# Performance work log

Measured on AMD Instinct MI355X. Metric: run time of the kernel, lower is better.

## Reference

```python
import jax, jax.numpy as jnp
import numpy as np

B, N, D = 2, 4096, 512   # batch, tokens (64x64 latent), query_dim
H, DH = 8, 64            # heads, dim_head; inner_dim = H*DH = 512


def setup_inputs() -> dict:
    key = jax.random.key(0)
    ks = jax.random.split(key, 6)
    s = lambda fan_in: 1.0 / np.sqrt(fan_in)
    x = jax.random.normal(ks[0], (B, N, D), dtype=jnp.float32)
    Wq = jax.random.uniform(ks[1], (D, H * DH), jnp.float32, -s(D), s(D))
    Wk = jax.random.uniform(ks[2], (D, H * DH), jnp.float32, -s(D), s(D))
    Wv = jax.random.uniform(ks[3], (D, H * DH), jnp.float32, -s(D), s(D))
    Wo = jax.random.uniform(ks[4], (H * DH, D), jnp.float32, -s(H * DH), s(H * DH))
    bo = jax.random.uniform(ks[5], (D,), jnp.float32, -s(H * DH), s(H * DH))
    return {"x": x, "Wq": Wq, "Wk": Wk, "Wv": Wv, "Wo": Wo, "bo": bo}


def reference(x, Wq, Wk, Wv, Wo, bo):
    # Self-attention (context = x). Projections (no bias).
    q = x @ Wq  # [B, N, H*DH]
    k = x @ Wk
    v = x @ Wv
    split = lambda t: t.reshape(B, N, H, DH).transpose(0, 2, 1, 3)  # [B, H, N, DH]
    q, k, v = split(q), split(k), split(v)
    scale = DH ** -0.5
    # fp32 upcast for scores (ATTN_PRECISION == 'fp32' path)
    sim = jnp.einsum('bhid,bhjd->bhij', q.astype(jnp.float32), k.astype(jnp.float32)) * scale
    attn = jax.nn.softmax(sim, axis=-1).astype(v.dtype)
    out = jnp.einsum('bhij,bhjd->bhid', attn, v)           # [B, H, N, DH]
    out = out.transpose(0, 2, 1, 3).reshape(B, N, H * DH)  # [B, N, H*DH]
    return out @ Wo + bo  # to_out Linear (dropout=0)
```

## Files before the change

kernel.cpp:

```cpp
#include <hip/hip_runtime.h>
#include <hip/hip_bf16.h>
#include <stdint.h>


typedef short short8 __attribute__((ext_vector_type(8)));
typedef float f32x4 __attribute__((ext_vector_type(4)));
typedef float f32x16 __attribute__((ext_vector_type(16)));

#define QK_SCALE 0.18033688011112042f
#define M3(a,b,c) fmaxf(fmaxf((a),(b)),(c))

static __device__ __forceinline__ unsigned short f32_to_bf16(float f) {
    union { float f; uint32_t u; } v; v.f = f;
    uint32_t u = v.u;
    u += 0x7FFFu + ((u >> 16) & 1u);
    return (unsigned short)(u >> 16);
}

static __device__ __forceinline__ uint32_t cvt_pk_bf16(float lo, float hi) {
    uint32_t r;
    asm("v_cvt_pk_bf16_f32 %0, %1, %2" : "=v"(r) : "v"(lo), "v"(hi));
    return r;
}

static __device__ __forceinline__ int swz(int row, int byte_in_row) {
    return row * 128 + (byte_in_row ^ ((row & 7) << 4));
}

static __device__ __forceinline__ void gload16(const void* g, void* l) {
    __builtin_amdgcn_global_load_lds(
        (const __attribute__((address_space(1))) unsigned int*)g,
        (__attribute__((address_space(3))) unsigned int*)l, 16, 0, 0);
}

union PAU { uint32_t d[4]; short8 v; };

__global__ __launch_bounds__(256) void convert_weights(
    const float* __restrict__ Wq, const float* __restrict__ Wk,
    const float* __restrict__ Wv, const float* __restrict__ Wo,
    unsigned short* __restrict__ wt)
{
    __shared__ float lds[64][65];
    const int mat = blockIdx.z;
    const float* W = (mat == 0) ? Wq : (mat == 1) ? Wk : (mat == 2) ? Wv : Wo;
    const float scale = (mat == 0) ? QK_SCALE : 1.0f;
    unsigned short* out = wt + (size_t)mat * 512 * 512;
    const int k0 = blockIdx.y * 64, n0 = blockIdx.x * 64;
    for (int i = 0; i < 16; i++) {
        int idx = threadIdx.x + i * 256;
        int kl = idx >> 6, nl = idx & 63;
        lds[kl][nl] = W[(size_t)(k0 + kl) * 512 + n0 + nl];
    }
    __syncthreads();
    for (int i = 0; i < 16; i++) {
        int idx = threadIdx.x + i * 256;
        int nr = idx >> 6, kc = idx & 63;
        out[(size_t)(n0 + nr) * 512 + k0 + kc] = f32_to_bf16(lds[kc][nr] * scale);
    }
}

__global__ __launch_bounds__(256) void convert_x(
    const float* __restrict__ x, unsigned short* __restrict__ xbf)
{
    const int idx = (blockIdx.x * 256 + threadIdx.x) * 8;
    float4 f0 = *reinterpret_cast<const float4*>(x + idx);
    float4 f1 = *reinterpret_cast<const float4*>(x + idx + 4);
    short8 v;
    v[0] = (short)f32_to_bf16(f0.x); v[1] = (short)f32_to_bf16(f0.y);
    v[2] = (short)f32_to_bf16(f0.z); v[3] = (short)f32_to_bf16(f0.w);
    v[4] = (short)f32_to_bf16(f1.x); v[5] = (short)f32_to_bf16(f1.y);
    v[6] = (short)f32_to_bf16(f1.z); v[7] = (short)f32_to_bf16(f1.w);
    *reinterpret_cast<short8*>(xbf + idx) = v;
}

__global__ __launch_bounds__(256, 2) void proj_gemm(
    const unsigned short* __restrict__ xbf,
    const unsigned short* __restrict__ wt,
    unsigned short* __restrict__ q_ws,
    unsigned short* __restrict__ k_ws,
    unsigned short* __restrict__ vt_ws)
{
    __shared__ __attribute__((aligned(16))) char smem[65536];
    const int which = blockIdx.z;
    const unsigned short* W = wt + (size_t)which * 512 * 512;
    const int m0 = blockIdx.y * 128, n0 = blockIdx.x * 128;
    const int tid = threadIdx.x, lane = tid & 63, wid = tid >> 6;
    const int wm = (wid >> 1) * 64, wn = (wid & 1) * 64;
    const int rsub = lane >> 3;
    const int cb = ((lane & 7) ^ rsub) << 4;

    f32x4 acc[4][4];
#pragma unroll
    for (int i = 0; i < 4; i++)
#pragma unroll
        for (int j = 0; j < 4; j++) acc[i][j] = (f32x4){0.f, 0.f, 0.f, 0.f};

#define PSTAGE(KT, BUF)                                                           \
    {                                                                             \
        const int kk0_ = (KT) * 64;                                               \
        _Pragma("unroll")                                                         \
        for (int cj = 0; cj < 4; cj++) {                                          \
            const int chunk = wid * 4 + cj;                                       \
            const int row = chunk * 8 + rsub;                                     \
            gload16((const char*)xbf + ((size_t)(m0 + row) * 512 + kk0_) * 2 + cb,\
                    smem + (BUF) * 32768 + chunk * 1024);                         \
            gload16((const char*)W + ((size_t)(n0 + row) * 512 + kk0_) * 2 + cb,  \
                    smem + (BUF) * 32768 + 16384 + chunk * 1024);                 \
        }                                                                         \
    }

    PSTAGE(0, 0);
    __syncthreads();

    for (int kt = 0; kt < 8; kt++) {
        const int cur = kt & 1;
        if (kt + 1 < 8) PSTAGE(kt + 1, cur ^ 1);
        unsigned short* ldsA = (unsigned short*)(smem + cur * 32768);
        unsigned short* ldsB = ldsA + 8192;
#pragma unroll
        for (int ks = 0; ks < 2; ks++) {
            const int kb = ks * 64 + (lane >> 4) * 16;
            short8 a[4], b[4];
#pragma unroll
            for (int m = 0; m < 4; m++)
                a[m] = *reinterpret_cast<short8*>(ldsA + (swz(wm + m * 16 + (lane & 15), kb) >> 1));
#pragma unroll
            for (int n = 0; n < 4; n++)
                b[n] = *reinterpret_cast<short8*>(ldsB + (swz(wn + n * 16 + (lane & 15), kb) >> 1));
            __builtin_amdgcn_s_setprio(1);
#pragma unroll
            for (int m = 0; m < 4; m++)
#pragma unroll
                for (int n = 0; n < 4; n++)
                    acc[m][n] = __builtin_amdgcn_mfma_f32_16x16x32_bf16(a[m], b[n], acc[m][n], 0, 0, 0);
            __builtin_amdgcn_s_setprio(0);
        }
        __syncthreads();
    }
#pragma unroll
    for (int m = 0; m < 4; m++)
#pragma unroll
        for (int n = 0; n < 4; n++)
#pragma unroll
            for (int r = 0; r < 4; r++) {
                int mr = m0 + wm + m * 16 + (lane >> 4) * 4 + r;
                int nc = n0 + wn + n * 16 + (lane & 15);
                unsigned short hv = f32_to_bf16(acc[m][n][r]);
                int b = mr >> 12, tok = mr & 4095;
                int h = nc >> 6, d = nc & 63;
                size_t bh = (size_t)(b * 8 + h);
                if (which == 2) {
                    vt_ws[(bh * 64 + d) * 4096 + tok] = hv;
                } else {
                    unsigned short* dst = (which == 0) ? q_ws : k_ws;
                    dst[(bh * 4096 + tok) * 64 + d] = hv;
                }
            }
}

__global__ __launch_bounds__(512, 4) void attn_kernel(
    const unsigned short* __restrict__ q_ws,
    const unsigned short* __restrict__ k_ws,
    const unsigned short* __restrict__ vt_ws,
    unsigned short* __restrict__ o_ws)
{
    __shared__ __attribute__((aligned(16))) char smem[65536];
    const int bh = blockIdx.y;
    const int q0 = blockIdx.x * 128;
    const int tid = threadIdx.x, lane = tid & 63, wid = tid >> 6;
    const int g = wid >> 2, sw = wid & 3;
    const int lo = lane & 31, hi = lane >> 5;
    const unsigned short* Qb = q_ws + (size_t)bh * 4096 * 64;
    const unsigned short* Kb = k_ws + (size_t)bh * 4096 * 64 + (size_t)g * 2048 * 64;
    const unsigned short* Vb = vt_ws + (size_t)bh * 64 * 4096 + g * 2048;

    char* gbase = smem + g * 32768;

    short8 qf[4];
    const int qrow = q0 + sw * 32 + lo;
#pragma unroll
    for (int s = 0; s < 4; s++)
        qf[s] = *reinterpret_cast<const short8*>(Qb + (size_t)qrow * 64 + s * 16 + hi * 8);

    f32x16 zv;
#pragma unroll
    for (int i = 0; i < 16; i++) zv[i] = 0.f;
    f32x16 acc[2];
    acc[0] = zv; acc[1] = zv;
    float m_run = -3e38f, l_run = 0.f;

    const int rsub = lane >> 3;
    const int cb = ((lane & 7) ^ rsub) << 4;

#define STAGE(TT, BUF)                                                          \
    {                                                                           \
        const int kv0_ = (TT) * 64;                                             \
        _Pragma("unroll")                                                       \
        for (int j = 0; j < 2; j++) {                                           \
            const int chunk = sw * 2 + j;                                       \
            const int row0 = chunk * 8;                                         \
            gload16((const char*)Kb + (size_t)(kv0_ + row0 + rsub) * 128 + cb,  \
                    gbase + (BUF) * 16384 + chunk * 1024);                      \
            gload16((const char*)Vb + (size_t)(row0 + rsub) * 8192 +            \
                        (size_t)kv0_ * 2 + cb,                                  \
                    gbase + (BUF) * 16384 + 8192 + chunk * 1024);               \
        }                                                                       \
    }

    STAGE(0, 0);
    __syncthreads();

    for (int t = 0; t < 32; t++) {
        const int cur = t & 1;
        if (t + 1 < 32) STAGE(t + 1, cur ^ 1);
        unsigned short* ldsK = (unsigned short*)(gbase + cur * 16384);
        unsigned short* ldsV = ldsK + 4096;

        f32x16 p[2];
        p[0] = zv; p[1] = zv;
        __builtin_amdgcn_s_setprio(1);
#pragma unroll
        for (int tt = 0; tt < 2; tt++)
#pragma unroll
            for (int s = 0; s < 4; s++) {
                short8 kf = *reinterpret_cast<short8*>(&ldsK[swz(tt * 32 + lo, s * 32 + hi * 16) >> 1]);
                p[tt] = __builtin_amdgcn_mfma_f32_32x32x16_bf16(kf, qf[s], p[tt], 0, 0, 0);
            }
        __builtin_amdgcn_s_setprio(0);

        float pm;
        {
            float a0 = M3(p[0][0], p[0][1], p[0][2]);
            float b0 = M3(p[0][3], p[0][4], p[0][5]);
            float c0 = M3(p[0][6], p[0][7], p[0][8]);
            float d0 = M3(p[0][9], p[0][10], p[0][11]);
            float e0 = M3(p[0][12], p[0][13], p[0][14]);
            float a1 = M3(p[1][0], p[1][1], p[1][2]);
            float b1 = M3(p[1][3], p[1][4], p[1][5]);
            float c1 = M3(p[1][6], p[1][7], p[1][8]);
            float d1 = M3(p[1][9], p[1][10], p[1][11]);
            float e1 = M3(p[1][12], p[1][13], p[1][14]);
            float f0 = fmaxf(p[0][15], p[1][15]);
            float x0 = M3(a0, b0, c0), x1 = M3(d0, e0, f0), x2 = M3(a1, b1, c1), x3 = M3(d1, e1, x1);
            pm = M3(x0, x2, x3);
        }
        pm = fmaxf(pm, __shfl_xor(pm, 32, 64));
        if (!__all(pm <= m_run + 8.0f)) {
            float mn = fmaxf(m_run, pm);
            float scl = __builtin_amdgcn_exp2f(m_run - mn);
            acc[0] *= scl; acc[1] *= scl;
            l_run *= scl;
            m_run = mn;
        }
        float s0 = 0.f, s1 = 0.f, s2 = 0.f, s3 = 0.f;
#pragma unroll
        for (int tt = 0; tt < 2; tt++)
#pragma unroll
            for (int i = 0; i < 16; i += 4) {
                float e0 = __builtin_amdgcn_exp2f(p[tt][i] - m_run);
                float e1 = __builtin_amdgcn_exp2f(p[tt][i + 1] - m_run);
                float e2 = __builtin_amdgcn_exp2f(p[tt][i + 2] - m_run);
                float e3 = __builtin_amdgcn_exp2f(p[tt][i + 3] - m_run);
                p[tt][i] = e0; p[tt][i + 1] = e1; p[tt][i + 2] = e2; p[tt][i + 3] = e3;
                s0 += e0; s1 += e1; s2 += e2; s3 += e3;
            }
        float ps = (s0 + s1) + (s2 + s3);
        ps += __shfl_xor(ps, 32, 64);
        l_run += ps;

        short8 pa[4];
#pragma unroll
        for (int tt = 0; tt < 2; tt++) {
            uint32_t w0 = cvt_pk_bf16(p[tt][0],  p[tt][1]);
            uint32_t w1 = cvt_pk_bf16(p[tt][2],  p[tt][3]);
            uint32_t w2 = cvt_pk_bf16(p[tt][4],  p[tt][5]);
            uint32_t w3 = cvt_pk_bf16(p[tt][6],  p[tt][7]);
            uint32_t w4 = cvt_pk_bf16(p[tt][8],  p[tt][9]);
            uint32_t w5 = cvt_pk_bf16(p[tt][10], p[tt][11]);
            uint32_t w6 = cvt_pk_bf16(p[tt][12], p[tt][13]);
            uint32_t w7 = cvt_pk_bf16(p[tt][14], p[tt][15]);
            auto r02 = __builtin_amdgcn_permlane32_swap(w0, w2, false, false);
            auto r13 = __builtin_amdgcn_permlane32_swap(w1, w3, false, false);
            auto r46 = __builtin_amdgcn_permlane32_swap(w4, w6, false, false);
            auto r57 = __builtin_amdgcn_permlane32_swap(w5, w7, false, false);
            PAU ua, ub;
            ua.d[0] = r02[0]; ua.d[1] = r13[0]; ua.d[2] = r02[1]; ua.d[3] = r13[1];
            ub.d[0] = r46[0]; ub.d[1] = r57[0]; ub.d[2] = r46[1]; ub.d[3] = r57[1];
            pa[2 * tt]     = ua.v;
            pa[2 * tt + 1] = ub.v;
        }

        __builtin_amdgcn_s_setprio(1);
#pragma unroll
        for (int dt = 0; dt < 2; dt++)
#pragma unroll
            for (int s = 0; s < 4; s++) {
                short8 vf = *reinterpret_cast<short8*>(&ldsV[swz(dt * 32 + lo, s * 32 + hi * 16) >> 1]);
                acc[dt] = __builtin_amdgcn_mfma_f32_32x32x16_bf16(vf, pa[s], acc[dt], 0, 0, 0);
            }
        __builtin_amdgcn_s_setprio(0);

        __syncthreads();
    }

    float* accbuf = (float*)smem;
    float* mlbuf  = (float*)(smem + 32768);
    if (g == 0) {
        float* ab = accbuf + sw * 2048;
#pragma unroll
        for (int dt = 0; dt < 2; dt++)
#pragma unroll
            for (int r = 0; r < 16; r++) {
                int d = dt * 32 + (r & 3) + 8 * (r >> 2) + 4 * hi;
                ab[d * 32 + lo] = acc[dt][r];
            }
        if (hi == 0) {
            mlbuf[sw * 64 + lo] = m_run;
            mlbuf[sw * 64 + 32 + lo] = l_run;
        }
    }
    __syncthreads();
    if (g == 1) {
        float m0 = mlbuf[sw * 64 + lo], l0 = mlbuf[sw * 64 + 32 + lo];
        float mn = fmaxf(m0, m_run);
        float a0 = __builtin_amdgcn_exp2f(m0 - mn);
        float a1 = __builtin_amdgcn_exp2f(m_run - mn);
        float rl = __builtin_amdgcn_rcpf(a0 * l0 + a1 * l_run);
        const float* ab = accbuf + sw * 2048;
        char* eb = smem + 33792 + sw * 4096;
#pragma unroll
        for (int dt = 0; dt < 2; dt++)
#pragma unroll
            for (int r = 0; r < 16; r++) {
                int d = dt * 32 + (r & 3) + 8 * (r >> 2) + 4 * hi;
                float o = (a0 * ab[d * 32 + lo] + a1 * acc[dt][r]) * rl;
                *(unsigned short*)(eb + swz(lo, d * 2)) = f32_to_bf16(o);
            }
        const int b = bh >> 3, h = bh & 7;
#pragma unroll
        for (int j = 0; j < 4; j++) {
            int c = lane + 64 * j;
            int row = c >> 3, cc = c & 7;
            short8 v = *reinterpret_cast<short8*>(eb + swz(row, cc * 16));
            int tok = q0 + sw * 32 + row;
            *reinterpret_cast<short8*>(o_ws + ((size_t)(b * 4096 + tok)) * 512 + h * 64 + cc * 8) = v;
        }
    }
}

__global__ __launch_bounds__(256, 2) void out_gemm(
    const unsigned short* __restrict__ o_ws,
    const unsigned short* __restrict__ wot,
    const float* __restrict__ bo,
    float* __restrict__ out)
{
    __shared__ __attribute__((aligned(16))) char smem[65536];
    const int m0 = blockIdx.y * 128, n0 = blockIdx.x * 128;
    const int tid = threadIdx.x, lane = tid & 63, wid = tid >> 6;
    const int wm = (wid >> 1) * 64, wn = (wid & 1) * 64;
    const int rsub = lane >> 3;
    const int cb = ((lane & 7) ^ rsub) << 4;

    f32x4 acc[4][4];
#pragma unroll
    for (int i = 0; i < 4; i++)
#pragma unroll
        for (int j = 0; j < 4; j++) acc[i][j] = (f32x4){0.f, 0.f, 0.f, 0.f};

#define OSTAGE(KT, BUF)                                                            \
    {                                                                              \
        const int kk0_ = (KT) * 64;                                                \
        _Pragma("unroll")                                                          \
        for (int cj = 0; cj < 4; cj++) {                                           \
            const int chunk = wid * 4 + cj;                                        \
            const int row = chunk * 8 + rsub;                                      \
            gload16((const char*)o_ws + ((size_t)(m0 + row) * 512 + kk0_) * 2 + cb,\
                    smem + (BUF) * 32768 + chunk * 1024);                          \
            gload16((const char*)wot + ((size_t)(n0 + row) * 512 + kk0_) * 2 + cb, \
                    smem + (BUF) * 32768 + 16384 + chunk * 1024);                  \
        }                                                                          \
    }

    OSTAGE(0, 0);
    __syncthreads();

    for (int kt = 0; kt < 8; kt++) {
        const int cur = kt & 1;
        if (kt + 1 < 8) OSTAGE(kt + 1, cur ^ 1);
        unsigned short* ldsA = (unsigned short*)(smem + cur * 32768);
        unsigned short* ldsB = ldsA + 8192;
#pragma unroll
        for (int ks = 0; ks < 2; ks++) {
            const int kb = ks * 64 + (lane >> 4) * 16;
            short8 a[4], b[4];
#pragma unroll
            for (int m = 0; m < 4; m++)
                a[m] = *reinterpret_cast<short8*>(ldsA + (swz(wm + m * 16 + (lane & 15), kb) >> 1));
#pragma unroll
            for (int n = 0; n < 4; n++)
                b[n] = *reinterpret_cast<short8*>(ldsB + (swz(wn + n * 16 + (lane & 15), kb) >> 1));
            __builtin_amdgcn_s_setprio(1);
#pragma unroll
            for (int m = 0; m < 4; m++)
#pragma unroll
                for (int n = 0; n < 4; n++)
                    acc[m][n] = __builtin_amdgcn_mfma_f32_16x16x32_bf16(a[m], b[n], acc[m][n], 0, 0, 0);
            __builtin_amdgcn_s_setprio(0);
        }
        __syncthreads();
    }
#pragma unroll
    for (int n = 0; n < 4; n++) {
        const int nc = n0 + wn + n * 16 + (lane & 15);
        const float bias = bo[nc];
#pragma unroll
        for (int m = 0; m < 4; m++)
#pragma unroll
            for (int r = 0; r < 4; r++) {
                int mr = m0 + wm + m * 16 + (lane >> 4) * 4 + r;
                out[(size_t)mr * 512 + nc] = acc[m][n][r] + bias;
            }
    }
}

extern "C" void kernel_launch(void* const* d_in, const int* in_sizes, int n_in,
                              void* d_out, int out_size, void* d_ws, size_t ws_size,
                              hipStream_t stream)
{
    const float* x  = (const float*)d_in[0];
    const float* Wq = (const float*)d_in[1];
    const float* Wk = (const float*)d_in[2];
    const float* Wv = (const float*)d_in[3];
    const float* Wo = (const float*)d_in[4];
    const float* bo = (const float*)d_in[5];
    float* out = (float*)d_out;

    char* ws = (char*)d_ws;
    unsigned short* wt    = (unsigned short*)(ws);
    unsigned short* q_ws  = (unsigned short*)(ws + (size_t)(2)  * 1024 * 1024);
    unsigned short* k_ws  = (unsigned short*)(ws + (size_t)(10) * 1024 * 1024);
    unsigned short* vt_ws = (unsigned short*)(ws + (size_t)(18) * 1024 * 1024);
    unsigned short* xbf   = (unsigned short*)(ws + (size_t)(26) * 1024 * 1024);
    unsigned short* o_ws  = xbf;

    convert_weights<<<dim3(8, 8, 4), 256, 0, stream>>>(Wq, Wk, Wv, Wo, wt);
    convert_x<<<dim3(2048), 256, 0, stream>>>(x, xbf);
    proj_gemm<<<dim3(4, 64, 3), 256, 0, stream>>>(xbf, wt, q_ws, k_ws, vt_ws);
    attn_kernel<<<dim3(32, 16), 512, 0, stream>>>(q_ws, k_ws, vt_ws, o_ws);
    out_gemm<<<dim3(4, 64), 256, 0, stream>>>(o_ws, wt + (size_t)3 * 512 * 512, bo, out);
}
```

Measured before the change: 140.2 us.

## Process two 32-row query tiles per wave to reuse K/V fragments

Each wave now handles 64 query rows (two 32-row sub-tiles) instead of 32, so every K and V fragment read from LDS feeds two MFMAs. The block covers 256 queries and the grid becomes 256 one-dimensional blocks, with a remapped block-to-(bh, q0) order that interleaves heads. This halves K/V global and LDS traffic per query but doubles accumulator and score registers, lowering launch bounds occupancy from 4 to 2 blocks per CU. There are also only 256 blocks, which may underfill the GPU's compute units.

```diff
diff --git a/kernel.cpp b/kernel.cpp
--- a/kernel.cpp
+++ b/kernel.cpp
@@ -158,15 +158,132 @@
             }
 }
 
-__global__ __launch_bounds__(512, 4) void attn_kernel(
+static __device__ __forceinline__ void softmax_step(
+    f32x16* p, float& m_run, float& l_run, f32x16* acc, short8* pa)
+{
+    float pm;
+    {
+        float a0 = M3(p[0][0], p[0][1], p[0][2]);
+        float b0 = M3(p[0][3], p[0][4], p[0][5]);
+        float c0 = M3(p[0][6], p[0][7], p[0][8]);
+        float d0 = M3(p[0][9], p[0][10], p[0][11]);
+        float e0 = M3(p[0][12], p[0][13], p[0][14]);
+        float a1 = M3(p[1][0], p[1][1], p[1][2]);
+        float b1 = M3(p[1][3], p[1][4], p[1][5]);
+        float c1 = M3(p[1][6], p[1][7], p[1][8]);
+        float d1 = M3(p[1][9], p[1][10], p[1][11]);
+        float e1 = M3(p[1][12], p[1][13], p[1][14]);
+        float f0 = fmaxf(p[0][15], p[1][15]);
+        float x0 = M3(a0, b0, c0), x1 = M3(d0, e0, f0), x2 = M3(a1, b1, c1), x3 = M3(d1, e1, x1);
+        pm = M3(x0, x2, x3);
+    }
+    pm = fmaxf(pm, __shfl_xor(pm, 32, 64));
+    if (!__all(pm <= m_run + 8.0f)) {
+        float mn = fmaxf(m_run, pm);
+        float scl = __builtin_amdgcn_exp2f(m_run - mn);
+        acc[0] *= scl; acc[1] *= scl;
+        l_run *= scl;
+        m_run = mn;
+    }
+    float s0 = 0.f, s1 = 0.f, s2 = 0.f, s3 = 0.f;
+#pragma unroll
+    for (int tt = 0; tt < 2; tt++)
+#pragma unroll
+        for (int i = 0; i < 16; i += 4) {
+            float e0 = __builtin_amdgcn_exp2f(p[tt][i] - m_run);
+            float e1 = __builtin_amdgcn_exp2f(p[tt][i + 1] - m_run);
+            float e2 = __builtin_amdgcn_exp2f(p[tt][i + 2] - m_run);
+            float e3 = __builtin_amdgcn_exp2f(p[tt][i + 3] - m_run);
+            p[tt][i] = e0; p[tt][i + 1] = e1; p[tt][i + 2] = e2; p[tt][i + 3] = e3;
+            s0 += e0; s1 += e1; s2 += e2; s3 += e3;
+        }
+    float ps = (s0 + s1) + (s2 + s3);
+    ps += __shfl_xor(ps, 32, 64);
+    l_run += ps;
+
+#pragma unroll
+    for (int tt = 0; tt < 2; tt++) {
+        uint32_t w0 = cvt_pk_bf16(p[tt][0],  p[tt][1]);
+        uint32_t w1 = cvt_pk_bf16(p[tt][2],  p[tt][3]);
+        uint32_t w2 = cvt_pk_bf16(p[tt][4],  p[tt][5]);
+        uint32_t w3 = cvt_pk_bf16(p[tt][6],  p[tt][7]);
+        uint32_t w4 = cvt_pk_bf16(p[tt][8],  p[tt][9]);
+        uint32_t w5 = cvt_pk_bf16(p[tt][10], p[tt][11]);
+        uint32_t w6 = cvt_pk_bf16(p[tt][12], p[tt][13]);
+        uint32_t w7 = cvt_pk_bf16(p[tt][14], p[tt][15]);
+        auto r02 = __builtin_amdgcn_permlane32_swap(w0, w2, false, false);
+        auto r13 = __builtin_amdgcn_permlane32_swap(w1, w3, false, false);
+        auto r46 = __builtin_amdgcn_permlane32_swap(w4, w6, false, false);
+        auto r57 = __builtin_amdgcn_permlane32_swap(w5, w7, false, false);
+        PAU ua, ub;
+        ua.d[0] = r02[0]; ua.d[1] = r13[0]; ua.d[2] = r02[1]; ua.d[3] = r13[1];
+        ub.d[0] = r46[0]; ub.d[1] = r57[0]; ub.d[2] = r46[1]; ub.d[3] = r57[1];
+        pa[2 * tt]     = ua.v;
+        pa[2 * tt + 1] = ub.v;
+    }
+}
+
+static __device__ __forceinline__ void merge_store(
+    f32x16 a0, f32x16 a1, float m_run, float l_run, int eoff,
+    char* smem, int q0, int sw, int g, int lane, int bh,
+    unsigned short* __restrict__ o_ws)
+{
+    const int lo = lane & 31, hi = lane >> 5;
+    float* accbuf = (float*)smem;
+    float* mlbuf  = (float*)(smem + 32768);
+    __syncthreads();
+    if (g == 0) {
+        float* ab = accbuf + sw * 2048;
+#pragma unroll
+        for (int r = 0; r < 16; r++) {
+            int d0 = (r & 3) + 8 * (r >> 2) + 4 * hi;
+            ab[d0 * 32 + lo] = a0[r];
+            ab[(d0 + 32) * 32 + lo] = a1[r];
+        }
+        if (hi == 0) {
+            mlbuf[sw * 64 + lo] = m_run;
+            mlbuf[sw * 64 + 32 + lo] = l_run;
+        }
+    }
+    __syncthreads();
+    if (g == 1) {
+        float m0 = mlbuf[sw * 64 + lo], l0 = mlbuf[sw * 64 + 32 + lo];
+        float mn = fmaxf(m0, m_run);
+        float c0 = __builtin_amdgcn_exp2f(m0 - mn);
+        float c1 = __builtin_amdgcn_exp2f(m_run - mn);
+        float rl = __builtin_amdgcn_rcpf(c0 * l0 + c1 * l_run);
+        const float* ab = accbuf + sw * 2048;
+        char* eb = smem + 33792 + sw * 4096;
+#pragma unroll
+        for (int r = 0; r < 16; r++) {
+            int d0 = (r & 3) + 8 * (r >> 2) + 4 * hi;
+            float o0 = (c0 * ab[d0 * 32 + lo] + c1 * a0[r]) * rl;
+            float o1 = (c0 * ab[(d0 + 32) * 32 + lo] + c1 * a1[r]) * rl;
+            *(unsigned short*)(eb + swz(lo, d0 * 2)) = f32_to_bf16(o0);
+            *(unsigned short*)(eb + swz(lo, (d0 + 32) * 2)) = f32_to_bf16(o1);
+        }
+        const int b = bh >> 3, h = bh & 7;
+#pragma unroll
+        for (int j = 0; j < 4; j++) {
+            int c = lane + 64 * j;
+            int row = c >> 3, cc = c & 7;
+            short8 v = *reinterpret_cast<short8*>(eb + swz(row, cc * 16));
+            int tok = q0 + sw * 64 + eoff + row;
+            *reinterpret_cast<short8*>(o_ws + ((size_t)(b * 4096 + tok)) * 512 + h * 64 + cc * 8) = v;
+        }
+    }
+}
+
+__global__ __launch_bounds__(512, 2) void attn_kernel(
     const unsigned short* __restrict__ q_ws,
     const unsigned short* __restrict__ k_ws,
     const unsigned short* __restrict__ vt_ws,
     unsigned short* __restrict__ o_ws)
 {
     __shared__ __attribute__((aligned(16))) char smem[65536];
-    const int bh = blockIdx.y;
-    const int q0 = blockIdx.x * 128;
+    const int blk = blockIdx.x;
+    const int bh = (blk & 7) * 2 + (blk >> 7);
+    const int q0 = ((blk >> 3) & 15) * 256;
     const int tid = threadIdx.x, lane = tid & 63, wid = tid >> 6;
     const int g = wid >> 2, sw = wid & 3;
     const int lo = lane & 31, hi = lane >> 5;
@@ -176,18 +293,20 @@
 
     char* gbase = smem + g * 32768;
 
-    short8 qf[4];
-    const int qrow = q0 + sw * 32 + lo;
-#pragma unroll
-    for (int s = 0; s < 4; s++)
-        qf[s] = *reinterpret_cast<const short8*>(Qb + (size_t)qrow * 64 + s * 16 + hi * 8);
+    short8 qfA[4], qfB[4];
+    const int qrA = q0 + sw * 64 + lo;
+#pragma unroll
+    for (int s = 0; s < 4; s++) {
+        qfA[s] = *reinterpret_cast<const short8*>(Qb + (size_t)qrA * 64 + s * 16 + hi * 8);
+        qfB[s] = *reinterpret_cast<const short8*>(Qb + (size_t)(qrA + 32) * 64 + s * 16 + hi * 8);
+    }
 
     f32x16 zv;
 #pragma unroll
     for (int i = 0; i < 16; i++) zv[i] = 0.f;
-    f32x16 acc[2];
-    acc[0] = zv; acc[1] = zv;
-    float m_run = -3e38f, l_run = 0.f;
+    f32x16 accA[2], accB[2];
+    accA[0] = zv; accA[1] = zv; accB[0] = zv; accB[1] = zv;
+    float mA = -3e38f, lA = 0.f, mB = -3e38f, lB = 0.f;
 
     const int rsub = lane >> 3;
     const int cb = ((lane & 7) ^ rsub) << 4;
@@ -216,79 +335,22 @@
         unsigned short* ldsK = (unsigned short*)(gbase + cur * 16384);
         unsigned short* ldsV = ldsK + 4096;
 
-        f32x16 p[2];
-        p[0] = zv; p[1] = zv;
+        f32x16 pA[2], pB[2];
+        pA[0] = zv; pA[1] = zv; pB[0] = zv; pB[1] = zv;
         __builtin_amdgcn_s_setprio(1);
 #pragma unroll
         for (int tt = 0; tt < 2; tt++)
 #pragma unroll
             for (int s = 0; s < 4; s++) {
                 short8 kf = *reinterpret_cast<short8*>(&ldsK[swz(tt * 32 + lo, s * 32 + hi * 16) >> 1]);
-                p[tt] = __builtin_amdgcn_mfma_f32_32x32x16_bf16(kf, qf[s], p[tt], 0, 0, 0);
+                pA[tt] = __builtin_amdgcn_mfma_f32_32x32x16_bf16(kf, qfA[s], pA[tt], 0, 0, 0);
+                pB[tt] = __builtin_amdgcn_mfma_f32_32x32x16_bf16(kf, qfB[s], pB[tt], 0, 0, 0);
             }
         __builtin_amdgcn_s_setprio(0);
 
-        float pm;
-        {
-            float a0 = M3(p[0][0], p[0][1], p[0][2]);
-            float b0 = M3(p[0][3], p[0][4], p[0][5]);
-            float c0 = M3(p[0][6], p[0][7], p[0][8]);
-            float d0 = M3(p[0][9], p[0][10], p[0][11]);
-            float e0 = M3(p[0][12], p[0][13], p[0][14]);
-            float a1 = M3(p[1][0], p[1][1], p[1][2]);
-            float b1 = M3(p[1][3], p[1][4], p[1][5]);
-            float c1 = M3(p[1][6], p[1][7], p[1][8]);
-            float d1 = M3(p[1][9], p[1][10], p[1][11]);
-            float e1 = M3(p[1][12], p[1][13], p[1][14]);
-            float f0 = fmaxf(p[0][15], p[1][15]);
-            float x0 = M3(a0, b0, c0), x1 = M3(d0, e0, f0), x2 = M3(a1, b1, c1), x3 = M3(d1, e1, x1);
-            pm = M3(x0, x2, x3);
-        }
-        pm = fmaxf(pm, __shfl_xor(pm, 32, 64));
-        if (!__all(pm <= m_run + 8.0f)) {
-            float mn = fmaxf(m_run, pm);
-            float scl = __builtin_amdgcn_exp2f(m_run - mn);
-            acc[0] *= scl; acc[1] *= scl;
-            l_run *= scl;
-            m_run = mn;
-        }
-        float s0 = 0.f, s1 = 0.f, s2 = 0.f, s3 = 0.f;
-#pragma unroll
-        for (int tt = 0; tt < 2; tt++)
-#pragma unroll
-            for (int i = 0; i < 16; i += 4) {
-                float e0 = __builtin_amdgcn_exp2f(p[tt][i] - m_run);
-                float e1 = __builtin_amdgcn_exp2f(p[tt][i + 1] - m_run);
-                float e2 = __builtin_amdgcn_exp2f(p[tt][i + 2] - m_run);
-                float e3 = __builtin_amdgcn_exp2f(p[tt][i + 3] - m_run);
-                p[tt][i] = e0; p[tt][i + 1] = e1; p[tt][i + 2] = e2; p[tt][i + 3] = e3;
-                s0 += e0; s1 += e1; s2 += e2; s3 += e3;
-            }
-        float ps = (s0 + s1) + (s2 + s3);
-        ps += __shfl_xor(ps, 32, 64);
-        l_run += ps;
-
-        short8 pa[4];
-#pragma unroll
-        for (int tt = 0; tt < 2; tt++) {
-            uint32_t w0 = cvt_pk_bf16(p[tt][0],  p[tt][1]);
-            uint32_t w1 = cvt_pk_bf16(p[tt][2],  p[tt][3]);
-            uint32_t w2 = cvt_pk_bf16(p[tt][4],  p[tt][5]);
-            uint32_t w3 = cvt_pk_bf16(p[tt][6],  p[tt][7]);
-            uint32_t w4 = cvt_pk_bf16(p[tt][8],  p[tt][9]);
-            uint32_t w5 = cvt_pk_bf16(p[tt][10], p[tt][11]);
-            uint32_t w6 = cvt_pk_bf16(p[tt][12], p[tt][13]);
-            uint32_t w7 = cvt_pk_bf16(p[tt][14], p[tt][15]);
-            auto r02 = __builtin_amdgcn_permlane32_swap(w0, w2, false, false);
-            auto r13 = __builtin_amdgcn_permlane32_swap(w1, w3, false, false);
-            auto r46 = __builtin_amdgcn_permlane32_swap(w4, w6, false, false);
-            auto r57 = __builtin_amdgcn_permlane32_swap(w5, w7, false, false);
-            PAU ua, ub;
-            ua.d[0] = r02[0]; ua.d[1] = r13[0]; ua.d[2] = r02[1]; ua.d[3] = r13[1];
-            ub.d[0] = r46[0]; ub.d[1] = r57[0]; ub.d[2] = r46[1]; ub.d[3] = r57[1];
-            pa[2 * tt]     = ua.v;
-            pa[2 * tt + 1] = ub.v;
-        }
+        short8 paA[4], paB[4];
+        softmax_step(pA, mA, lA, accA, paA);
+        softmax_step(pB, mB, lB, accB, paB);
 
         __builtin_amdgcn_s_setprio(1);
 #pragma unroll
@@ -296,56 +358,16 @@
 #pragma unroll
             for (int s = 0; s < 4; s++) {
                 short8 vf = *reinterpret_cast<short8*>(&ldsV[swz(dt * 32 + lo, s * 32 + hi * 16) >> 1]);
-                acc[dt] = __builtin_amdgcn_mfma_f32_32x32x16_bf16(vf, pa[s], acc[dt], 0, 0, 0);
+                accA[dt] = __builtin_amdgcn_mfma_f32_32x32x16_bf16(vf, paA[s], accA[dt], 0, 0, 0);
+                accB[dt] = __builtin_amdgcn_mfma_f32_32x32x16_bf16(vf, paB[s], accB[dt], 0, 0, 0);
             }
         __builtin_amdgcn_s_setprio(0);
 
         __syncthreads();
     }
 
-    float* accbuf = (float*)smem;
-    float* mlbuf  = (float*)(smem + 32768);
-    if (g == 0) {
-        float* ab = accbuf + sw * 2048;
-#pragma unroll
-        for (int dt = 0; dt < 2; dt++)
-#pragma unroll
-            for (int r = 0; r < 16; r++) {
-                int d = dt * 32 + (r & 3) + 8 * (r >> 2) + 4 * hi;
-                ab[d * 32 + lo] = acc[dt][r];
-            }
-        if (hi == 0) {
-            mlbuf[sw * 64 + lo] = m_run;
-            mlbuf[sw * 64 + 32 + lo] = l_run;
-        }
-    }
-    __syncthreads();
-    if (g == 1) {
-        float m0 = mlbuf[sw * 64 + lo], l0 = mlbuf[sw * 64 + 32 + lo];
-        float mn = fmaxf(m0, m_run);
-        float a0 = __builtin_amdgcn_exp2f(m0 - mn);
-        float a1 = __builtin_amdgcn_exp2f(m_run - mn);
-        float rl = __builtin_amdgcn_rcpf(a0 * l0 + a1 * l_run);
-        const float* ab = accbuf + sw * 2048;
-        char* eb = smem + 33792 + sw * 4096;
-#pragma unroll
-        for (int dt = 0; dt < 2; dt++)
-#pragma unroll
-            for (int r = 0; r < 16; r++) {
-                int d = dt * 32 + (r & 3) + 8 * (r >> 2) + 4 * hi;
-                float o = (a0 * ab[d * 32 + lo] + a1 * acc[dt][r]) * rl;
-                *(unsigned short*)(eb + swz(lo, d * 2)) = f32_to_bf16(o);
-            }
-        const int b = bh >> 3, h = bh & 7;
-#pragma unroll
-        for (int j = 0; j < 4; j++) {
-            int c = lane + 64 * j;
-            int row = c >> 3, cc = c & 7;
-            short8 v = *reinterpret_cast<short8*>(eb + swz(row, cc * 16));
-            int tok = q0 + sw * 32 + row;
-            *reinterpret_cast<short8*>(o_ws + ((size_t)(b * 4096 + tok)) * 512 + h * 64 + cc * 8) = v;
-        }
-    }
+    merge_store(accA[0], accA[1], mA, lA, 0,  smem, q0, sw, g, lane, bh, o_ws);
+    merge_store(accB[0], accB[1], mB, lB, 32, smem, q0, sw, g, lane, bh, o_ws);
 }
 
 __global__ __launch_bounds__(256, 2) void out_gemm(
@@ -446,6 +468,6 @@
     convert_weights<<<dim3(8, 8, 4), 256, 0, stream>>>(Wq, Wk, Wv, Wo, wt);
     convert_x<<<dim3(2048), 256, 0, stream>>>(x, xbf);
     proj_gemm<<<dim3(4, 64, 3), 256, 0, stream>>>(xbf, wt, q_ws, k_ws, vt_ws);
-    attn_kernel<<<dim3(32, 16), 512, 0, stream>>>(q_ws, k_ws, vt_ws, o_ws);
+    attn_kernel<<<dim3(256), 512, 0, stream>>>(q_ws, k_ws, vt_ws, o_ws);
     out_gemm<<<dim3(4, 64), 256, 0, stream>>>(o_ws, wt + (size_t)3 * 512 * 512, bo, out);
 }
```

Result: no change. 138.1 us (-1.5%).
